# Kernel optimization log

Hardware: AMD Instinct MI355X
Metric: run time of the kernel (lower is better)

Reference implementation:

```python
import jax, jax.numpy as jnp
import numpy as np

B, S, H = 2, 4096, 1024  # batch, seq_len, hidden_size (= all_head_size)


def setup_inputs() -> dict:
    key = jax.random.key(0)
    ks = jax.random.split(key, 7)
    sc = 1.0 / np.sqrt(H)
    return {
        "hidden_states": jax.random.normal(ks[0], (B, S, H), dtype=jnp.float32),
        "Wq": jax.random.normal(ks[1], (H, H), dtype=jnp.float32) * sc,
        "bq": jnp.zeros((H,), dtype=jnp.float32),
        "Wk": jax.random.normal(ks[2], (H, H), dtype=jnp.float32) * sc,
        "bk": jnp.zeros((H,), dtype=jnp.float32),
        "Wv": jax.random.normal(ks[3], (H, H), dtype=jnp.float32) * sc,
        "bv": jnp.zeros((H,), dtype=jnp.float32),
    }


def reference(hidden_states, Wq, bq, Wk, bk, Wv, bv):
    # QKV projections (weights stored as [in, out] = W.T of torch Linear)
    q = hidden_states @ Wq + bq  # [B,S,H]
    k = hidden_states @ Wk + bk
    v = hidden_states @ Wv + bv
    # Raw attention: no head split, no 1/sqrt(d) scaling (faithful to source)
    scores = jnp.einsum("bqh,bkh->bqk", q, k)  # [B,S,S]
    probs = jax.nn.softmax(scores, axis=-1)
    context = jnp.einsum("bqk,bkh->bqh", probs, v)  # [B,S,H]
    return context
```

## Files before the change

### kernel.cpp

```cpp
#include <hip/hip_runtime.h>
#include <stdint.h>

typedef __attribute__((ext_vector_type(8))) short short8;
typedef __attribute__((ext_vector_type(8))) _Float16 half8;
typedef __attribute__((ext_vector_type(4))) float f32x4;

__device__ __forceinline__ unsigned short f2h(float x) {
  _Float16 h = (_Float16)x;
  return __builtin_bit_cast(unsigned short, h);
}
__device__ __forceinline__ float h2f(unsigned short u) {
  return (float)__builtin_bit_cast(_Float16, u);
}

#define GLOAD16(gsrc, ldst)                                              \
  __builtin_amdgcn_global_load_lds(                                      \
      (const __attribute__((address_space(1))) void*)(gsrc),             \
      (__attribute__((address_space(3))) void*)(ldst), 16, 0, 0)

#define VM(N) asm volatile("s_waitcnt vmcnt(" #N ")" ::: "memory")
#define BARSYNC __builtin_amdgcn_s_barrier()
#define LGKM0                                                \
  do {                                                       \
    asm volatile("s_waitcnt lgkmcnt(0)" ::: "memory");       \
    __builtin_amdgcn_sched_barrier(0);                       \
  } while (0)

__global__ __launch_bounds__(256) void split_pair_f16_kernel(
    const float* __restrict__ in, unsigned short* __restrict__ h,
    unsigned short* __restrict__ l) {
  size_t i = (size_t)blockIdx.x * 256 + threadIdx.x;
  float4 a = ((const float4*)in)[2 * i];
  float4 b = ((const float4*)in)[2 * i + 1];
  ushort4 h0 = make_ushort4(f2h(a.x), f2h(a.y), f2h(a.z), f2h(a.w));
  ushort4 h1 = make_ushort4(f2h(b.x), f2h(b.y), f2h(b.z), f2h(b.w));
  ((ushort4*)h)[2 * i] = h0;
  ((ushort4*)h)[2 * i + 1] = h1;
  ((ushort4*)l)[2 * i] = make_ushort4(
      f2h(a.x - h2f(h0.x)), f2h(a.y - h2f(h0.y)),
      f2h(a.z - h2f(h0.z)), f2h(a.w - h2f(h0.w)));
  ((ushort4*)l)[2 * i + 1] = make_ushort4(
      f2h(b.x - h2f(h1.x)), f2h(b.y - h2f(h1.y)),
      f2h(b.z - h2f(h1.z)), f2h(b.w - h2f(h1.w)));
}

__global__ __launch_bounds__(256) void transpose_f16x3_kernel(
    const float* __restrict__ Wq, const float* __restrict__ Wk,
    const float* __restrict__ Wv, unsigned short* __restrict__ hT) {
  __shared__ float tile[32][33];
  const float* W = blockIdx.z == 0 ? Wq : blockIdx.z == 1 ? Wk : Wv;
  unsigned short* dst = hT + (size_t)blockIdx.z * 1024 * 1024;
  int r = threadIdx.x >> 3;
  int c = (threadIdx.x & 7) * 4;
  int k0 = blockIdx.y * 32, n0 = blockIdx.x * 32;
  float4 v = *(const float4*)&W[(size_t)(k0 + r) * 1024 + n0 + c];
  tile[r][c] = v.x; tile[r][c + 1] = v.y; tile[r][c + 2] = v.z; tile[r][c + 3] = v.w;
  __syncthreads();
  size_t o = (size_t)(n0 + r) * 1024 + k0 + c;
  *(ushort4*)&dst[o] = make_ushort4(f2h(tile[c + 0][r]), f2h(tile[c + 1][r]),
                                    f2h(tile[c + 2][r]), f2h(tile[c + 3][r]));
}

__global__ __launch_bounds__(256) void transpose_v_kernel(
    const unsigned short* __restrict__ Vs, unsigned short* __restrict__ vT) {
  __shared__ unsigned short tile[32][36];
  int r = threadIdx.x >> 3;
  int c = (threadIdx.x & 7) * 4;
  int col0 = blockIdx.x * 32;
  int row0 = blockIdx.y * 32;
  ushort4 v = *(const ushort4*)&Vs[(size_t)(row0 + r) * 1024 + col0 + c];
  tile[r][c] = v.x; tile[r][c + 1] = v.y; tile[r][c + 2] = v.z; tile[r][c + 3] = v.w;
  __syncthreads();
  ushort4 o = make_ushort4(tile[c + 0][r], tile[c + 1][r],
                           tile[c + 2][r], tile[c + 3][r]);
  *(ushort4*)&vT[(size_t)(col0 + r) * 8192 + row0 + c] = o;
}

__global__ __launch_bounds__(512, 2) void qkv_kernel(
    const unsigned short* __restrict__ Ah, const unsigned short* __restrict__ Al,
    const unsigned short* __restrict__ WT, const float* __restrict__ bq,
    const float* __restrict__ bk, const float* __restrict__ bv,
    unsigned short* __restrict__ qh, unsigned short* __restrict__ kh,
    unsigned short* __restrict__ vS) {
  __shared__ __align__(16) char smem[4 * 40 * 1024];
  constexpr int lda = 1024, ldb = 1024, K = 1024;
  const int t = threadIdx.x, wid = t >> 6, lane = t & 63;
  const int waveM = wid >> 2, waveN = wid & 3;
  const int lr0 = lane & 15, lk0 = (lane >> 4) * 8;
  const int m0 = blockIdx.y * 128, n0 = blockIdx.x * 384;

  const unsigned short* slot_src[5];
#pragma unroll
  for (int s = 0; s < 5; ++s) {
    int si = 5 * wid + s;
    const unsigned short* p;
    if (si < 8)       p = Ah + (size_t)(m0 + si * 16 + lr0) * lda + lk0;
    else if (si < 16) p = Al + (size_t)(m0 + (si - 8) * 16 + lr0) * lda + lk0;
    else              p = WT + (size_t)(n0 + (si - 16) * 16 + lr0) * ldb + lk0;
    slot_src[s] = p;
  }

  const int NTILES = K >> 5;
  f32x4 acc[4][6] = {};

#pragma unroll
  for (int tt = 0; tt < 3; ++tt)
#pragma unroll
    for (int s = 0; s < 5; ++s)
      GLOAD16(slot_src[s] + (size_t)tt * 32,
              smem + tt * 40960 + (5 * wid + s) * 1024);
  VM(10);
  BARSYNC;
  __builtin_amdgcn_sched_barrier(0);

  for (int tile = 0; tile < NTILES; ++tile) {
    const int cur = tile & 3, nxt = (tile + 3) & 3;
    const bool do_stage = (tile + 3) < NTILES;
    const bool t2f = (tile + 2) < NTILES;
    const char* cb = smem + cur * 40960;
    char* nb = smem + nxt * 40960;
    half8 bf[6];
#pragma unroll
    for (int p = 0; p < 4; ++p) {
      const int mg = waveM * 4 + p;
      half8 ahf = *(const half8*)(cb + mg * 1024 + lane * 16);
      half8 alf = *(const half8*)(cb + (8 + mg) * 1024 + lane * 16);
      if (p == 0) {
#pragma unroll
        for (int j = 0; j < 6; ++j) {
          int ng = waveN * 6 + j;
          bf[j] = *(const half8*)(cb + (16 + ng) * 1024 + lane * 16);
        }
      }
      if (do_stage) {
        if (p == 0) {
          GLOAD16(slot_src[0] + (size_t)(tile + 3) * 32, nb + (5 * wid + 0) * 1024);
          GLOAD16(slot_src[1] + (size_t)(tile + 3) * 32, nb + (5 * wid + 1) * 1024);
        } else {
          const int slot = p + 1;
          GLOAD16(slot_src[slot] + (size_t)(tile + 3) * 32,
                  nb + (5 * wid + slot) * 1024);
        }
      }
      __builtin_amdgcn_s_setprio(1);
#pragma unroll
      for (int j = 0; j < 6; ++j) {
        f32x4 c = acc[p][j];
        c = __builtin_amdgcn_mfma_f32_16x16x32_f16(ahf, bf[j], c, 0, 0, 0);
        c = __builtin_amdgcn_mfma_f32_16x16x32_f16(alf, bf[j], c, 0, 0, 0);
        acc[p][j] = c;
      }
      __builtin_amdgcn_s_setprio(0);
      if (p < 3) __builtin_amdgcn_s_barrier();
    }
    if (tile + 1 < NTILES) {
      if (do_stage) VM(10);
      else if (t2f) VM(5);
      else VM(0);
      BARSYNC;
      __builtin_amdgcn_sched_barrier(0);
    }
  }

  const int or0 = (lane >> 4) * 4;
#pragma unroll
  for (int mm = 0; mm < 4; ++mm)
#pragma unroll
    for (int j = 0; j < 6; ++j)
#pragma unroll
      for (int r = 0; r < 4; ++r) {
        int row = m0 + waveM * 64 + mm * 16 + or0 + r;
        int gc = n0 + waveN * 96 + j * 16 + lr0;
        int slab = gc >> 10;
        int col = gc & 1023;
        float x = acc[mm][j][r];
        if (slab == 0) {
          qh[(size_t)row * 1024 + col] = f2h(x + bq[col]);
        } else if (slab == 1) {
          kh[(size_t)row * 1024 + col] = f2h(x + bk[col]);
        } else {
          vS[(size_t)row * 1024 + col] = f2h(x + bv[col]);
        }
      }
}

#define ST8(h, T, bufb)                                                   \
  do {                                                                    \
    const unsigned short* _s = ssrc[h] + (size_t)(T) * 64;                \
    char* _d = smem + (bufb) * 65536 + sdst[h];                           \
    GLOAD16(_s, _d);                                                      \
    GLOAD16(_s + 32, _d + 1024);                                          \
  } while (0)

#define RDA(bufb, qr)                                                     \
  _Pragma("unroll") for (int _i = 0; _i < 4; ++_i)                        \
  _Pragma("unroll") for (int _kk = 0; _kk < 2; ++_kk)                     \
      areg[_i][_kk] = *(const half8*)(smem + (bufb) * 65536 +             \
          ((waveM * 8 + (qr) * 4 + _i) * 2 + _kk) * 1024 + lane * 16);

#define RDB(bufb, qc)                                                     \
  _Pragma("unroll") for (int _j = 0; _j < 2; ++_j)                        \
  _Pragma("unroll") for (int _kk = 0; _kk < 2; ++_kk)                     \
      breg[_j][_kk] = *(const half8*)(smem + (bufb) * 65536 + 32768 +     \
          ((waveN * 4 + (qc) * 2 + _j) * 2 + _kk) * 1024 + lane * 16);

#define MM16(qr, qc)                                                      \
  __builtin_amdgcn_s_setprio(1);                                          \
  _Pragma("unroll") for (int _i = 0; _i < 4; ++_i)                        \
  _Pragma("unroll") for (int _j = 0; _j < 2; ++_j)                        \
  _Pragma("unroll") for (int _kk = 0; _kk < 2; ++_kk)                     \
      acc[(qr) * 4 + _i][(qc) * 2 + _j] =                                 \
          __builtin_amdgcn_mfma_f32_16x16x32_f16(                         \
              areg[_i][_kk], breg[_j][_kk],                               \
              acc[(qr) * 4 + _i][(qc) * 2 + _j], 0, 0, 0);                \
  __builtin_amdgcn_s_setprio(0);

__global__ __launch_bounds__(512, 2) void g8q_kernel(
    const unsigned short* __restrict__ Abase, size_t Astr, int lda,
    const unsigned short* __restrict__ Bbase, size_t Bstr, int ldb,
    float* __restrict__ outF, size_t Ostr, int ldo, int K) {
  __shared__ __align__(16) char smem[131072];
  const int t = threadIdx.x, wid = t >> 6, lane = t & 63;
  const int waveM = wid >> 2, waveN = wid & 3;
  const int lr0 = lane & 15, lk0 = (lane >> 4) * 8;
  const int m0 = blockIdx.y * 256, n0 = blockIdx.x * 256;
  const unsigned short* A = Abase + (size_t)blockIdx.z * Astr;
  const unsigned short* B = Bbase + (size_t)blockIdx.z * Bstr;
  float* out = outF + (size_t)blockIdx.z * Ostr;

  const int rgA0 = (wid & 3) + ((wid >> 2) << 3);
  const int rgA1 = rgA0 + 4;
  const int cgB0 = (wid & 1) + ((wid >> 1) << 2);
  const int cgB1 = cgB0 + 2;
  const unsigned short* ssrc[4];
  int sdst[4];
  ssrc[0] = A + (size_t)(m0 + rgA0 * 16 + lr0) * lda + lk0;
  ssrc[1] = A + (size_t)(m0 + rgA1 * 16 + lr0) * lda + lk0;
  ssrc[2] = B + (size_t)(n0 + cgB0 * 16 + lr0) * ldb + lk0;
  ssrc[3] = B + (size_t)(n0 + cgB1 * 16 + lr0) * ldb + lk0;
  sdst[0] = (rgA0 * 2) * 1024;
  sdst[1] = (rgA1 * 2) * 1024;
  sdst[2] = 32768 + (cgB0 * 2) * 1024;
  sdst[3] = 32768 + (cgB1 * 2) * 1024;

  const int NT = K >> 6, NT2 = NT >> 1;
  f32x4 acc[8][4] = {};
  half8 areg[4][2], breg[2][2];

  ST8(0, 0, 0); ST8(2, 0, 0); ST8(1, 0, 0); ST8(3, 0, 0);
  ST8(2, 1, 1); ST8(1, 1, 1); ST8(3, 1, 1);
  VM(6);
  BARSYNC;
  __builtin_amdgcn_sched_barrier(0);

#pragma unroll 1
  for (int it = 0; it < NT2; ++it) {
    const int tt = 2 * it;
    const bool s2 = (tt + 2) < NT;
    const bool s3 = (tt + 3) < NT;
    RDA(0, 0) RDB(0, 0)
    ST8(0, tt + 1, 1);
    BARSYNC; LGKM0; MM16(0, 0) BARSYNC;
    RDA(0, 1)
    if (s2) ST8(2, tt + 2, 0);
    BARSYNC; LGKM0; MM16(1, 0) BARSYNC;
    RDB(0, 1)
    if (s2) ST8(1, tt + 2, 0);
    BARSYNC; LGKM0; MM16(1, 1) BARSYNC;
    RDA(0, 0)
    if (s2) ST8(3, tt + 2, 0);
    BARSYNC; LGKM0; MM16(0, 1)
    if (s2) { VM(6); } else { VM(0); }
    BARSYNC;
    RDA(1, 0) RDB(1, 0)
    if (s2) ST8(0, tt + 2, 0);
    BARSYNC; LGKM0; MM16(0, 0) BARSYNC;
    RDA(1, 1)
    if (s3) ST8(2, tt + 3, 1);
    BARSYNC; LGKM0; MM16(1, 0) BARSYNC;
    RDB(1, 1)
    if (s3) ST8(1, tt + 3, 1);
    BARSYNC; LGKM0; MM16(1, 1) BARSYNC;
    RDA(1, 0)
    if (s3) ST8(3, tt + 3, 1);
    BARSYNC; LGKM0; MM16(0, 1)
    if (s3) { VM(6); }
    BARSYNC;
  }

  const int or0 = (lane >> 4) * 4;
#pragma unroll
  for (int mm = 0; mm < 8; ++mm)
#pragma unroll
    for (int cg = 0; cg < 4; ++cg)
#pragma unroll
      for (int r = 0; r < 4; ++r)
        out[(size_t)(m0 + waveM * 128 + mm * 16 + or0 + r) * ldo +
            (n0 + waveN * 64 + cg * 16 + lr0)] = acc[mm][cg][r];
}

__global__ __launch_bounds__(512, 2) void g1t_kernel(
    const unsigned short* __restrict__ Abase, size_t Astr, int lda,
    const unsigned short* __restrict__ Bbase, size_t Bstr, int ldb,
    float* __restrict__ outF, size_t Ostr, int ldo, int K) {
  __shared__ __align__(16) char smem[3 * 48 * 1024];
  const int t = threadIdx.x, wid = t >> 6, lane = t & 63;
  const int waveM = wid >> 2, waveN = wid & 3;
  const int lr0 = lane & 15, lk0 = (lane >> 4) * 8;
  const int m0 = blockIdx.y * 128, n0 = blockIdx.x * 256;
  const unsigned short* A = Abase + (size_t)blockIdx.z * Astr;
  const unsigned short* B = Bbase + (size_t)blockIdx.z * Bstr;
  float* out = outF + (size_t)blockIdx.z * Ostr;

  const unsigned short* slot_src[6];
#pragma unroll
  for (int s = 0; s < 6; ++s) {
    int si = 6 * wid + s;
    const unsigned short* p;
    if (si < 8)       p = A + (size_t)(m0 + si * 16 + lr0) * lda + lk0;
    else if (si < 16) p = A + (size_t)(m0 + (si - 8) * 16 + lr0) * lda + 32 + lk0;
    else if (si < 32) p = B + (size_t)(n0 + (si - 16) * 16 + lr0) * ldb + lk0;
    else              p = B + (size_t)(n0 + (si - 32) * 16 + lr0) * ldb + 32 + lk0;
    slot_src[s] = p;
  }

  const int NTILES = K >> 6;
  f32x4 acc[4][4] = {};

#pragma unroll
  for (int tt = 0; tt < 2; ++tt)
#pragma unroll
    for (int s = 0; s < 6; ++s)
      GLOAD16(slot_src[s] + (size_t)tt * 64,
              smem + tt * 49152 + (6 * wid + s) * 1024);
  VM(6);
  BARSYNC;
  __builtin_amdgcn_sched_barrier(0);

  for (int tile = 0; tile < NTILES; ++tile) {
    const int cur = tile % 3, nxt = (tile + 2) % 3;
    const bool do_stage = (tile + 2) < NTILES;
    const char* cb = smem + cur * 49152;
    char* nb = smem + nxt * 49152;
    half8 blo[4], bhi[4];
#pragma unroll
    for (int p = 0; p < 4; ++p) {
      const int mg = waveM * 4 + p;
      half8 alo = *(const half8*)(cb + mg * 1024 + lane * 16);
      half8 ahi = *(const half8*)(cb + (8 + mg) * 1024 + lane * 16);
      if (p == 0) {
#pragma unroll
        for (int j = 0; j < 4; ++j) {
          int ng = waveN * 4 + j;
          blo[j] = *(const half8*)(cb + (16 + ng) * 1024 + lane * 16);
          bhi[j] = *(const half8*)(cb + (32 + ng) * 1024 + lane * 16);
        }
      }
      if (do_stage && p < 3) {
#pragma unroll
        for (int s = 0; s < 2; ++s) {
          int slot = 2 * p + s;
          GLOAD16(slot_src[slot] + (size_t)(tile + 2) * 64,
                  nb + (6 * wid + slot) * 1024);
        }
      }
      __builtin_amdgcn_s_setprio(1);
#pragma unroll
      for (int j = 0; j < 4; ++j) {
        f32x4 c = acc[p][j];
        c = __builtin_amdgcn_mfma_f32_16x16x32_f16(alo, blo[j], c, 0, 0, 0);
        c = __builtin_amdgcn_mfma_f32_16x16x32_f16(ahi, bhi[j], c, 0, 0, 0);
        acc[p][j] = c;
      }
      __builtin_amdgcn_s_setprio(0);
    }
    if (tile + 1 < NTILES) {
      LGKM0;
      if (do_stage) VM(6); else VM(0);
      BARSYNC;
      __builtin_amdgcn_sched_barrier(0);
    }
  }

  const int or0 = (lane >> 4) * 4;
#pragma unroll
  for (int mm = 0; mm < 4; ++mm)
#pragma unroll
    for (int j = 0; j < 4; ++j)
#pragma unroll
      for (int r = 0; r < 4; ++r)
        out[(size_t)(m0 + waveM * 64 + mm * 16 + or0 + r) * ldo +
            (n0 + waveN * 64 + j * 16 + lr0)] = acc[mm][j][r];
}

__global__ __launch_bounds__(256) void softmax_rows_kernel(
    const float* Sm, unsigned short* P, int ncol, int pld) {
  const int t = threadIdx.x;
  const float* srow = Sm + (size_t)blockIdx.x * ncol;
  float4 v[4];
  float m = -3.4e38f;
#pragma unroll
  for (int i = 0; i < 4; ++i) {
    v[i] = ((const float4*)srow)[t + 256 * i];
    m = fmaxf(m, fmaxf(fmaxf(v[i].x, v[i].y), fmaxf(v[i].z, v[i].w)));
  }
#pragma unroll
  for (int off = 32; off >= 1; off >>= 1) m = fmaxf(m, __shfl_down(m, off));
  __shared__ float redm[4];
  if ((t & 63) == 0) redm[t >> 6] = m;
  __syncthreads();
  m = fmaxf(fmaxf(redm[0], redm[1]), fmaxf(redm[2], redm[3]));
  float s = 0.f;
#pragma unroll
  for (int i = 0; i < 4; ++i) {
    v[i].x = __expf(v[i].x - m);
    v[i].y = __expf(v[i].y - m);
    v[i].z = __expf(v[i].z - m);
    v[i].w = __expf(v[i].w - m);
    s += v[i].x + v[i].y + v[i].z + v[i].w;
  }
#pragma unroll
  for (int off = 32; off >= 1; off >>= 1) s += __shfl_down(s, off);
  __shared__ float reds[4];
  if ((t & 63) == 0) reds[t >> 6] = s;
  __syncthreads();
  s = reds[0] + reds[1] + reds[2] + reds[3];
  float inv = 1.f / s;
  unsigned short* prow = P + (size_t)blockIdx.x * pld;
#pragma unroll
  for (int i = 0; i < 4; ++i) {
    ushort4 o = make_ushort4(f2h(v[i].x * inv), f2h(v[i].y * inv),
                             f2h(v[i].z * inv), f2h(v[i].w * inv));
    ((ushort4*)prow)[t + 256 * i] = o;
  }
}

extern "C" void kernel_launch(void* const* d_in, const int* in_sizes, int n_in,
                              void* d_out, int out_size, void* d_ws, size_t ws_size,
                              hipStream_t stream) {
  const float* hs = (const float*)d_in[0];
  const float* Wq = (const float*)d_in[1];
  const float* bq = (const float*)d_in[2];
  const float* Wk = (const float*)d_in[3];
  const float* bk = (const float*)d_in[4];
  const float* Wv = (const float*)d_in[5];
  const float* bv = (const float*)d_in[6];
  float* out = (float*)d_out;

  constexpr int Ss = 4096, Hh = 1024;
  constexpr int Mm = 8192;
  constexpr size_t TOK = (size_t)Ss * Hh;
  char* ws = (char*)d_ws;
  const size_t MB = 1024 * 1024;

  unsigned short* qh = (unsigned short*)(ws + 0 * MB);
  unsigned short* kh = (unsigned short*)(ws + 16 * MB);
  unsigned short* vT = (unsigned short*)(ws + 32 * MB);
  char* rb = ws + 48 * MB;
  unsigned short* hs_h = (unsigned short*)(rb + 0 * MB);
  unsigned short* hs_l = (unsigned short*)(rb + 16 * MB);
  unsigned short* WT = (unsigned short*)(rb + 32 * MB);
  unsigned short* vS = (unsigned short*)(rb + 38 * MB);
  float* Sf = (float*)rb;

  const bool big = ws_size >= (size_t)176 * MB;

  split_pair_f16_kernel<<<dim3(Mm * Hh / 2048), 256, 0, stream>>>(hs, hs_h, hs_l);
  transpose_f16x3_kernel<<<dim3(32, 32, 3), 256, 0, stream>>>(Wq, Wk, Wv, WT);

  qkv_kernel<<<dim3(8, 64), 512, 0, stream>>>(
      hs_h, hs_l, WT, bq, bk, bv, qh, kh, vS);

  transpose_v_kernel<<<dim3(32, 256), 256, 0, stream>>>(vS, vT);

  if (big) {
    g8q_kernel<<<dim3(16, 16, 2), 512, 0, stream>>>(
        qh, TOK, Hh, kh, TOK, Hh, Sf, (size_t)Ss * Ss, Ss, Hh);
    softmax_rows_kernel<<<dim3(2 * Ss), 256, 0, stream>>>(
        Sf, (unsigned short*)Sf, Ss, 2 * Ss);
    g1t_kernel<<<dim3(4, 32, 2), 512, 0, stream>>>(
        (const unsigned short*)Sf, (size_t)Ss * 2 * Ss, 2 * Ss,
        vT, (size_t)Ss, Mm, out, TOK, Hh, Ss);
  } else {
    float* Sb = (float*)rb;
    unsigned short* Pb = (unsigned short*)(rb + 64 * MB);
    for (int b = 0; b < 2; ++b) {
      g8q_kernel<<<dim3(16, 16, 1), 512, 0, stream>>>(
          qh + b * TOK, 0, Hh, kh + b * TOK, 0, Hh, Sb, 0, Ss, Hh);
      softmax_rows_kernel<<<dim3(Ss), 256, 0, stream>>>(Sb, Pb, Ss, Ss);
      g1t_kernel<<<dim3(4, 32, 1), 512, 0, stream>>>(
          Pb, 0, Ss, vT + (size_t)b * Ss, 0, Mm, out + b * TOK, 0, Hh, Ss);
    }
  }
}
```

Measured before the change: 359.9 us.

## Restructure QKV GEMM into double-buffered 64-wide K tiles with quadrant pipelining

Replaces the 4-stage, 32-wide-K pipeline of the QKV projection kernel with a 2-buffer scheme using 64-wide K tiles (80KB per buffer). The inner loop is split into quadrant sub-steps, each interleaving LDS fragment reads, half-tile global-to-LDS staging and MFMA work, with barriers between them. The aim is to halve outer-loop iterations and barrier overhead per K step while overlapping loads with compute. In exchange it adds many more barriers per tile, depends on fine-grained vmcnt accounting, and leaves only two buffers for latency hiding.

```diff
diff --git a/kernel.cpp b/kernel.cpp
--- a/kernel.cpp
+++ b/kernel.cpp
@@ -76,90 +76,130 @@
   *(ushort4*)&vT[(size_t)(col0 + r) * 8192 + row0 + c] = o;
 }
 
-__global__ __launch_bounds__(512, 2) void qkv_kernel(
+#define QSTA0(T, bufb)                                                    \
+  _Pragma("unroll") for (int _c = 0; _c < 2; ++_c)                        \
+      GLOAD16(srcA[_c] + (size_t)(T) * 64,                                \
+              smem + (bufb) * 81920 + dstA[_c]);
+#define QSTA1(T, bufb)                                                    \
+  _Pragma("unroll") for (int _c = 0; _c < 2; ++_c)                        \
+      GLOAD16(srcA[_c] + 32768 + (size_t)(T) * 64,                        \
+              smem + (bufb) * 81920 + dstA[_c] + 4096);
+#define QSTB0(T, bufb)                                                    \
+  _Pragma("unroll") for (int _c = 0; _c < 3; ++_c)                        \
+      GLOAD16(srcB[_c] + (size_t)(T) * 64,                                \
+              smem + (bufb) * 81920 + dstB[_c]);
+#define QSTB1(T, bufb)                                                    \
+  _Pragma("unroll") for (int _c = 0; _c < 3; ++_c)                        \
+      GLOAD16(srcB[_c] + 49152 + (size_t)(T) * 64,                        \
+              smem + (bufb) * 81920 + dstB[_c] + 6144);
+
+#define QRDA(bufb, qr)                                                    \
+  _Pragma("unroll") for (int _i = 0; _i < 2; ++_i)                        \
+  _Pragma("unroll") for (int _kk = 0; _kk < 2; ++_kk) {                   \
+    const int _rg = waveM * 4 + (qr) * 2 + _i;                            \
+    ahf[_i][_kk] = *(const half8*)(smem + (bufb) * 81920 +                \
+        (_rg * 2 + _kk) * 1024 + lane * 16);                              \
+    alf[_i][_kk] = *(const half8*)(smem + (bufb) * 81920 + 16384 +        \
+        (_rg * 2 + _kk) * 1024 + lane * 16);                              \
+  }
+#define QRDB(bufb, qc)                                                    \
+  _Pragma("unroll") for (int _j = 0; _j < 3; ++_j)                        \
+  _Pragma("unroll") for (int _kk = 0; _kk < 2; ++_kk) {                   \
+    const int _cg = waveN * 6 + (qc) * 3 + _j;                            \
+    bfr[_j][_kk] = *(const half8*)(smem + (bufb) * 81920 + 32768 +        \
+        (_cg * 2 + _kk) * 1024 + lane * 16);                              \
+  }
+#define QMM(qr, qc)                                                       \
+  __builtin_amdgcn_s_setprio(1);                                          \
+  _Pragma("unroll") for (int _kk = 0; _kk < 2; ++_kk)                     \
+  _Pragma("unroll") for (int _i = 0; _i < 2; ++_i)                        \
+  _Pragma("unroll") for (int _j = 0; _j < 3; ++_j) {                      \
+    f32x4 _cc = acc[(qr) * 2 + _i][(qc) * 3 + _j];                        \
+    _cc = __builtin_amdgcn_mfma_f32_16x16x32_f16(ahf[_i][_kk],            \
+          bfr[_j][_kk], _cc, 0, 0, 0);                                    \
+    _cc = __builtin_amdgcn_mfma_f32_16x16x32_f16(alf[_i][_kk],            \
+          bfr[_j][_kk], _cc, 0, 0, 0);                                    \
+    acc[(qr) * 2 + _i][(qc) * 3 + _j] = _cc;                              \
+  }                                                                       \
+  __builtin_amdgcn_s_setprio(0);
+
+__global__ __launch_bounds__(512, 2) void qkv8_kernel(
     const unsigned short* __restrict__ Ah, const unsigned short* __restrict__ Al,
     const unsigned short* __restrict__ WT, const float* __restrict__ bq,
     const float* __restrict__ bk, const float* __restrict__ bv,
     unsigned short* __restrict__ qh, unsigned short* __restrict__ kh,
     unsigned short* __restrict__ vS) {
-  __shared__ __align__(16) char smem[4 * 40 * 1024];
-  constexpr int lda = 1024, ldb = 1024, K = 1024;
+  __shared__ __align__(16) char smem[2 * 80 * 1024];
   const int t = threadIdx.x, wid = t >> 6, lane = t & 63;
   const int waveM = wid >> 2, waveN = wid & 3;
   const int lr0 = lane & 15, lk0 = (lane >> 4) * 8;
   const int m0 = blockIdx.y * 128, n0 = blockIdx.x * 384;
 
-  const unsigned short* slot_src[5];
-#pragma unroll
-  for (int s = 0; s < 5; ++s) {
-    int si = 5 * wid + s;
-    const unsigned short* p;
-    if (si < 8)       p = Ah + (size_t)(m0 + si * 16 + lr0) * lda + lk0;
-    else if (si < 16) p = Al + (size_t)(m0 + (si - 8) * 16 + lr0) * lda + lk0;
-    else              p = WT + (size_t)(n0 + (si - 16) * 16 + lr0) * ldb + lk0;
-    slot_src[s] = p;
-  }
-
-  const int NTILES = K >> 5;
+  const unsigned short* srcA[2];
+  int dstA[2];
+#pragma unroll
+  for (int c = 0; c < 2; ++c) {
+    int idx = 2 * wid + c;
+    int rgI = idx >> 2, ty = (idx >> 1) & 1, kk = idx & 1;
+    int rg = (rgI & 1) + ((rgI >> 1) << 2);
+    const unsigned short* base = ty ? Al : Ah;
+    srcA[c] = base + (size_t)(m0 + rg * 16 + lr0) * 1024 + kk * 32 + lk0;
+    dstA[c] = ty * 16384 + (rg * 2 + kk) * 1024;
+  }
+  const unsigned short* srcB[3];
+  int dstB[3];
+#pragma unroll
+  for (int c = 0; c < 3; ++c) {
+    int idx = 3 * wid + c;
+    int cgI = idx >> 1, kk = idx & 1;
+    int cg = (cgI % 3) + (cgI / 3) * 6;
+    srcB[c] = WT + (size_t)(n0 + cg * 16 + lr0) * 1024 + kk * 32 + lk0;
+    dstB[c] = 32768 + (cg * 2 + kk) * 1024;
+  }
+
+  const int NT = 1024 >> 6, NT2 = NT >> 1;
   f32x4 acc[4][6] = {};
-
-#pragma unroll
-  for (int tt = 0; tt < 3; ++tt)
-#pragma unroll
-    for (int s = 0; s < 5; ++s)
-      GLOAD16(slot_src[s] + (size_t)tt * 32,
-              smem + tt * 40960 + (5 * wid + s) * 1024);
-  VM(10);
+  half8 ahf[2][2], alf[2][2], bfr[3][2];
+
+  QSTA0(0, 0) QSTB0(0, 0) QSTA1(0, 0) QSTB1(0, 0)
+  QSTB0(1, 1) QSTA1(1, 1) QSTB1(1, 1)
+  VM(8);
   BARSYNC;
   __builtin_amdgcn_sched_barrier(0);
 
-  for (int tile = 0; tile < NTILES; ++tile) {
-    const int cur = tile & 3, nxt = (tile + 3) & 3;
-    const bool do_stage = (tile + 3) < NTILES;
-    const bool t2f = (tile + 2) < NTILES;
-    const char* cb = smem + cur * 40960;
-    char* nb = smem + nxt * 40960;
-    half8 bf[6];
-#pragma unroll
-    for (int p = 0; p < 4; ++p) {
-      const int mg = waveM * 4 + p;
-      half8 ahf = *(const half8*)(cb + mg * 1024 + lane * 16);
-      half8 alf = *(const half8*)(cb + (8 + mg) * 1024 + lane * 16);
-      if (p == 0) {
-#pragma unroll
-        for (int j = 0; j < 6; ++j) {
-          int ng = waveN * 6 + j;
-          bf[j] = *(const half8*)(cb + (16 + ng) * 1024 + lane * 16);
-        }
-      }
-      if (do_stage) {
-        if (p == 0) {
-          GLOAD16(slot_src[0] + (size_t)(tile + 3) * 32, nb + (5 * wid + 0) * 1024);
-          GLOAD16(slot_src[1] + (size_t)(tile + 3) * 32, nb + (5 * wid + 1) * 1024);
-        } else {
-          const int slot = p + 1;
-          GLOAD16(slot_src[slot] + (size_t)(tile + 3) * 32,
-                  nb + (5 * wid + slot) * 1024);
-        }
-      }
-      __builtin_amdgcn_s_setprio(1);
-#pragma unroll
-      for (int j = 0; j < 6; ++j) {
-        f32x4 c = acc[p][j];
-        c = __builtin_amdgcn_mfma_f32_16x16x32_f16(ahf, bf[j], c, 0, 0, 0);
-        c = __builtin_amdgcn_mfma_f32_16x16x32_f16(alf, bf[j], c, 0, 0, 0);
-        acc[p][j] = c;
-      }
-      __builtin_amdgcn_s_setprio(0);
-      if (p < 3) __builtin_amdgcn_s_barrier();
-    }
-    if (tile + 1 < NTILES) {
-      if (do_stage) VM(10);
-      else if (t2f) VM(5);
-      else VM(0);
-      BARSYNC;
-      __builtin_amdgcn_sched_barrier(0);
-    }
+#pragma unroll 1
+  for (int it = 0; it < NT2; ++it) {
+    const int tt = 2 * it;
+    const bool s2 = (tt + 2) < NT;
+    const bool s3 = (tt + 3) < NT;
+    QRDA(0, 0) QRDB(0, 0)
+    QSTA0(tt + 1, 1)
+    BARSYNC; LGKM0; QMM(0, 0) BARSYNC;
+    QRDA(0, 1)
+    if (s2) QSTB0(tt + 2, 0)
+    BARSYNC; LGKM0; QMM(1, 0) BARSYNC;
+    QRDB(0, 1)
+    if (s2) QSTA1(tt + 2, 0)
+    BARSYNC; LGKM0; QMM(1, 1) BARSYNC;
+    QRDA(0, 0)
+    if (s2) QSTB1(tt + 2, 0)
+    BARSYNC; LGKM0; QMM(0, 1)
+    if (s2) { VM(8); } else { VM(0); }
+    BARSYNC;
+    QRDA(1, 0) QRDB(1, 0)
+    if (s2) QSTA0(tt + 2, 0)
+    BARSYNC; LGKM0; QMM(0, 0) BARSYNC;
+    QRDA(1, 1)
+    if (s3) QSTB0(tt + 3, 1)
+    BARSYNC; LGKM0; QMM(1, 0) BARSYNC;
+    QRDB(1, 1)
+    if (s3) QSTA1(tt + 3, 1)
+    BARSYNC; LGKM0; QMM(1, 1) BARSYNC;
+    QRDA(1, 0)
+    if (s3) QSTB1(tt + 3, 1)
+    BARSYNC; LGKM0; QMM(0, 1)
+    if (s3) { VM(8); }
+    BARSYNC;
   }
 
   const int or0 = (lane >> 4) * 4;
@@ -468,7 +508,7 @@
   split_pair_f16_kernel<<<dim3(Mm * Hh / 2048), 256, 0, stream>>>(hs, hs_h, hs_l);
   transpose_f16x3_kernel<<<dim3(32, 32, 3), 256, 0, stream>>>(Wq, Wk, Wv, WT);
 
-  qkv_kernel<<<dim3(8, 64), 512, 0, stream>>>(
+  qkv8_kernel<<<dim3(8, 64), 512, 0, stream>>>(
       hs_h, hs_l, WT, bq, bk, bv, qh, kh, vS);
 
   transpose_v_kernel<<<dim3(32, 256), 256, 0, stream>>>(vS, vT);
```

New measurement: 360.9 us. About the same (+0.3%).
